# Kernel tuning notes

Measured on AMD Instinct MI355X. Metric: run time of the kernel, lower is better.

Reference implementation:

```python
import jax, jax.numpy as jnp
import numpy as np

FISTA_ITER = 50
LAMBDA = 0.1
POWER_ITER = 100


def power_method(W):
    # Estimates c = largest eigenvalue of W^T W (squared spectral norm).
    # Torch code uses a random init vector; we use a fixed key for determinism.
    X0 = jax.random.normal(jax.random.key(1), (1, W.shape[1]), dtype=W.dtype)

    def body(i, carry):
        X, _ = carry
        X = (X @ W.T) @ W            # [1, m]
        nm = jnp.linalg.norm(X)
        return (X / nm, nm)

    _, nm = jax.lax.fori_loop(0, POWER_ITER, body, (X0, jnp.asarray(1.0, W.dtype)))
    return nm


def soft_threshold(X, lam):
    return jnp.sign(X) * jax.nn.relu(jnp.abs(X) - lam)


def fista(Y, W, lam, iters):
    c = power_method(W)
    eta = 1.0 / c
    Gamma0 = soft_threshold(Y @ (eta * W), lam)   # [B, m]
    Y_norm = jnp.linalg.norm(Y)
    t0 = jnp.asarray(1.0, Y.dtype)

    def step(carry, _):
        Gamma, Z, t = carry
        residual = Z @ W.T - Y                                   # [B, n]
        Gamma_new = soft_threshold(Z - eta * (residual @ W), lam / c)
        t_new = (1.0 + jnp.sqrt(1.0 + 4.0 * t ** 2)) / 2.0
        Z_new = Gamma_new + (t - 1.0) / t_new * (Gamma_new - Gamma)
        nrm = jnp.linalg.norm(residual) / Y_norm
        return (Gamma_new, Z_new, t_new), nrm

    (Gamma, _, _), norms = jax.lax.scan(step, (Gamma0, Gamma0, t0), None, length=iters)
    return Gamma, norms


def setup_inputs() -> dict:
    key = jax.random.key(0)
    k1, k2 = jax.random.split(key)
    Y = jax.random.normal(k1, (8192, 784), dtype=jnp.float32)
    W = jax.random.normal(k2, (784, 2048), dtype=jnp.float32)
    W = W / jnp.linalg.norm(W, axis=0, keepdims=True)  # NormDict
    return {"Y": Y, "W": W}


def reference(Y, W):
    Gamma, norms = fista(Y, W, LAMBDA, FISTA_ITER)
    X = Gamma @ W.T                  # reconstruction [B, 784]
    return (X, Gamma, norms)
```

## Files before the change

### kernel.cpp

```cpp
#include <hip/hip_runtime.h>
#include <math.h>

#define B_DIM   8192
#define N_DIM   784
#define NPAD    800
#define NROWS_W 1024
#define M_DIM   2048
#define XSZ     (B_DIM*N_DIM)
#define GSZ     (B_DIM*M_DIM)
#define NITER   50
#define PITER   100

typedef __attribute__((ext_vector_type(8))) short short8;
typedef __attribute__((ext_vector_type(4))) float floatx4;

__device__ __forceinline__ void async_ld16(const unsigned short* g, unsigned short* l){
  __builtin_amdgcn_global_load_lds(
      (const __attribute__((address_space(1))) unsigned int*)g,
      (__attribute__((address_space(3))) unsigned int*)l,
      16, 0, 0);
}

__device__ __forceinline__ unsigned rotl32(unsigned x, int d){ return (x<<d)|(x>>(32-d)); }

__device__ void threefry2x32(unsigned& v0, unsigned& v1){
  const unsigned ks0=0u, ks1=1u, ks2=0x1BD11BDBu;
  unsigned x0=v0+ks0, x1=v1+ks1;
#define RND(R) { x0+=x1; x1=rotl32(x1,R); x1^=x0; }
  RND(13) RND(15) RND(26) RND(6)
  x0+=ks1; x1+=ks2+1u;
  RND(17) RND(29) RND(16) RND(24)
  x0+=ks2; x1+=ks0+2u;
  RND(13) RND(15) RND(26) RND(6)
  x0+=ks0; x1+=ks1+3u;
  RND(17) RND(29) RND(16) RND(24)
  x0+=ks1; x1+=ks2+4u;
  RND(13) RND(15) RND(26) RND(6)
  x0+=ks2; x1+=ks0+5u;
#undef RND
  v0=x0; v1=x1;
}

__device__ float erfinv_f(float x){
  float w = -logf((1.0f-x)*(1.0f+x));
  float p;
  if (w < 5.0f){
    w -= 2.5f;
    p = 2.81022636e-08f;
    p = fmaf(p,w, 3.43273939e-07f);
    p = fmaf(p,w,-3.5233877e-06f);
    p = fmaf(p,w,-4.39150654e-06f);
    p = fmaf(p,w, 0.00021858087f);
    p = fmaf(p,w,-0.00125372503f);
    p = fmaf(p,w,-0.00417768164f);
    p = fmaf(p,w, 0.246640727f);
    p = fmaf(p,w, 1.50140941f);
  } else {
    w = sqrtf(w) - 3.0f;
    p = -0.000200214257f;
    p = fmaf(p,w, 0.000100950558f);
    p = fmaf(p,w, 0.00134934322f);
    p = fmaf(p,w,-0.00367342844f);
    p = fmaf(p,w, 0.00573950773f);
    p = fmaf(p,w,-0.0076224613f);
    p = fmaf(p,w, 0.00943887047f);
    p = fmaf(p,w, 1.00167406f);
    p = fmaf(p,w, 2.83297682f);
  }
  return p*x;
}

__device__ float bits_to_normal(unsigned b){
  unsigned fb = (b>>9) | 0x3f800000u;
  float u01 = __uint_as_float(fb) - 1.0f;
  const float lo = -0.99999994f;
  float u = u01*(1.0f - lo) + lo;
  u = fmaxf(lo, u);
  return 1.41421356237f * erfinv_f(u);
}

__global__ void setup_kernel(float* __restrict__ xbuf0, float* __restrict__ accs,
                             float* __restrict__ dbuf){
  int i = threadIdx.x;
  if (i < 64) accs[i] = 0.0f;
  if (i < 128) dbuf[i] = (i==0) ? 1.0f : 0.0f;
  unsigned v0 = (unsigned)i, v1 = (unsigned)(1024+i);
  threefry2x32(v0, v1);
  xbuf0[i]        = bits_to_normal(v0);
  xbuf0[1024 + i] = bits_to_normal(v1);
}

__device__ __forceinline__ unsigned short f2bf(float f){
  unsigned u = __float_as_uint(f);
  unsigned r = (u + 0x7fffu + ((u>>16)&1u)) >> 16;
  return (unsigned short)r;
}
__device__ __forceinline__ unsigned pack2(float a, float b){
  return (unsigned)f2bf(a) | ((unsigned)f2bf(b) << 16);
}
__device__ __forceinline__ float bf2f(unsigned short s){
  return __uint_as_float(((unsigned)s) << 16);
}

__global__ void conv_w(const float* __restrict__ W, unsigned short* __restrict__ Wbf){
  int i4 = (blockIdx.x*256 + threadIdx.x)*4;
  int row = i4 >> 11;
  uint2 p = make_uint2(0,0);
  if (row < N_DIM){
    float4 v = *(const float4*)(W + (size_t)row*M_DIM + (i4 & 2047));
    p.x = pack2(v.x, v.y); p.y = pack2(v.z, v.w);
  }
  *(uint2*)(Wbf + i4) = p;
}

__global__ void conv_y(const float* __restrict__ Y, unsigned short* __restrict__ Ybf){
  int row = blockIdx.x;
  int c4 = threadIdx.x*4;
  if (c4 >= NPAD) return;
  uint2 p = make_uint2(0,0);
  if (c4 < N_DIM){
    float4 v = *(const float4*)(Y + (size_t)row*N_DIM + c4);
    p.x = pack2(v.x, v.y); p.y = pack2(v.z, v.w);
  }
  *(uint2*)(Ybf + (size_t)row*NPAD + c4) = p;
}

__global__ void transpose_w(const float* __restrict__ W, unsigned short* __restrict__ WTbf){
  __shared__ float tile[32][33];
  int k0 = blockIdx.x*32;
  int j0 = blockIdx.y*32;
  int tx = threadIdx.x & 31, ty = threadIdx.x >> 5;
#pragma unroll
  for (int i=0;i<4;i++){
    int j = j0 + ty + 8*i;
    float v = (j < N_DIM) ? W[(size_t)j*M_DIM + k0 + tx] : 0.0f;
    tile[tx][ty+8*i] = v;
  }
  __syncthreads();
#pragma unroll
  for (int i=0;i<4;i++){
    int k = k0 + ty + 8*i;
    WTbf[(size_t)k*NPAD + j0 + tx] = f2bf(tile[ty+8*i][tx]);
  }
}

__global__ __launch_bounds__(256)
void compute_qp(const float* __restrict__ W, float* __restrict__ Qp){
  __shared__ float As2[64][33];
  __shared__ float Bs2[64][33];
  const int t = threadIdx.x;
  const int a0 = blockIdx.x*64, b0 = blockIdx.y*64;
  const int ty = t>>4, tx = t&15;
  float acc[4][4];
#pragma unroll
  for (int i=0;i<4;i++)
#pragma unroll
    for (int j=0;j<4;j++) acc[i][j]=0.0f;

  for (int k0=0; k0<M_DIM; k0+=32){
#pragma unroll
    for (int h=0; h<2; ++h){
      int row = h*32 + (t>>3);
      int kq  = (t&7)*4;
      float4 av = make_float4(0,0,0,0), bv = make_float4(0,0,0,0);
      if (a0+row < N_DIM) av = *(const float4*)(W + (size_t)(a0+row)*M_DIM + k0 + kq);
      if (b0+row < N_DIM) bv = *(const float4*)(W + (size_t)(b0+row)*M_DIM + k0 + kq);
      As2[row][kq]=av.x; As2[row][kq+1]=av.y; As2[row][kq+2]=av.z; As2[row][kq+3]=av.w;
      Bs2[row][kq]=bv.x; Bs2[row][kq+1]=bv.y; Bs2[row][kq+2]=bv.z; Bs2[row][kq+3]=bv.w;
    }
    __syncthreads();
#pragma unroll
    for (int kk=0; kk<32; ++kk){
      float a[4], b[4];
#pragma unroll
      for (int i=0;i<4;i++) a[i] = As2[ty*4+i][kk];
#pragma unroll
      for (int j=0;j<4;j++) b[j] = Bs2[tx*4+j][kk];
#pragma unroll
      for (int i=0;i<4;i++)
#pragma unroll
        for (int j=0;j<4;j++) acc[i][j] = fmaf(a[i], b[j], acc[i][j]);
    }
    __syncthreads();
  }
#pragma unroll
  for (int i=0;i<4;i++){
    int a = a0 + ty*4 + i;
    if (a >= N_DIM) continue;
#pragma unroll
    for (int j=0;j<4;j++){
      int b = b0 + tx*4 + j;
      if (b < N_DIM) Qp[(size_t)a*N_DIM + b] = acc[i][j];
    }
  }
}

__global__ void u0_kernel(const float* __restrict__ x0, const float* __restrict__ W,
                          float* __restrict__ u0){
  int wave = threadIdx.x>>6, lane = threadIdx.x&63;
  int j = blockIdx.x*4 + wave;
  const float* Wr = W + (size_t)j*M_DIM;
  float s = 0.0f;
  for (int k=lane; k<M_DIM; k+=64) s = fmaf(x0[k], Wr[k], s);
  for (int off=32; off>0; off>>=1) s += __shfl_down(s, off);
  if (lane==0) u0[j] = s;
}

__global__ void pm_qp(const float* __restrict__ vin, const float* __restrict__ din,
                      const float* __restrict__ Qp,
                      float* __restrict__ vout, float* __restrict__ dout){
  int wave = threadIdx.x>>6, lane = threadIdx.x&63;
  int j = blockIdx.x*4 + wave;
  float inv = 1.0f/sqrtf(*din);
  const float* Qr = Qp + (size_t)j*N_DIM;
  float s = 0.0f;
  for (int k=lane; k<N_DIM; k+=64) s = fmaf(vin[k], Qr[k], s);
  for (int off=32; off>0; off>>=1) s += __shfl_down(s, off);
  if (lane==0){
    float w = s * inv;
    vout[j] = w;
    atomicAdd(dout, w * vin[j] * inv);
  }
}

__global__ void finish_power2(const float* __restrict__ d100, const float* __restrict__ accs,
                              float* __restrict__ params){
  float c = sqrtf(*d100);
  params[0] = c;
  params[1] = 1.0f/c;
  params[2] = 0.1f/c;
  params[3] = sqrtf(accs[0]);
}

__global__ void sumsq_kernel(const float* __restrict__ v, int n, float* __restrict__ acc){
  __shared__ float red[256];
  int t = threadIdx.x;
  float s = 0.0f;
  for (int i = blockIdx.x*256 + t; i < n; i += gridDim.x*256){ float x = v[i]; s = fmaf(x,x,s); }
  red[t] = s; __syncthreads();
  for (int off=128; off>0; off>>=1){ if (t<off) red[t]+=red[t+off]; __syncthreads(); }
  if (t==0) atomicAdd(acc, red[0]);
}

__device__ __forceinline__ float softthr(float v, float th){
  float a = fmaxf(fabsf(v) - th, 0.0f);
  return copysignf(a, v);
}

template<int MODE>
__global__ __launch_bounds__(256)
void mfma_nt(const unsigned short* __restrict__ Abf,
             const unsigned short* __restrict__ Bbf,
             const float* __restrict__ Y,
             unsigned short* __restrict__ Rbf,
             float* __restrict__ X,
             float* __restrict__ nacc){
  __shared__ float4 smem4[2560];
  unsigned short* As0 = (unsigned short*)smem4;
  unsigned short* Bs0 = As0 + 64*32;
  unsigned short* As1 = Bs0 + 256*32;
  unsigned short* Bs1 = As1 + 64*32;
  float* fbuf = (float*)smem4;

  const int bid = blockIdx.x;
  const int g8  = bid & 7, w = bid >> 3;
  const int m0  = (g8*16 + (w>>2))*64;
  const int n0  = (w & 3)*256;

  const int t    = threadIdx.x;
  const int wave = t>>6, lane = t&63;
  const int wm2  = wave>>1, wn2 = wave&1;
  const int quad = lane>>4, l15 = lane&15;
  const int lrow = lane>>2;
  const int lks  = ((lane&3) ^ ((lrow>>1)&3))*8;
  const int ksw  = (quad ^ ((l15>>1)&3))*8;

  floatx4 acc[2][8];
#pragma unroll
  for (int i=0;i<2;i++)
#pragma unroll
    for (int j=0;j<8;j++) acc[i][j] = (floatx4)(0.0f);

  auto stage = [&](unsigned short* As, unsigned short* Bs, int k0){
    async_ld16(Abf + (size_t)(m0 + wave*16 + lrow)*M_DIM + k0 + lks, &As[wave*512]);
#pragma unroll
    for (int c=0; c<4; ++c){
      int chunk = wave*4 + c;
      async_ld16(Bbf + (size_t)(n0 + chunk*16 + lrow)*M_DIM + k0 + lks, &Bs[chunk*512]);
    }
  };

  stage(As0, Bs0, 0);
  __syncthreads();
  int cur = 0;
  for (int k0=0; k0<M_DIM; k0+=32, cur^=1){
    unsigned short* As = cur ? As1 : As0;
    unsigned short* Bs = cur ? Bs1 : Bs0;
    if (k0+32 < M_DIM) stage(cur ? As0 : As1, cur ? Bs0 : Bs1, k0+32);
    short8 af[2], bfr[8];
#pragma unroll
    for (int ti=0; ti<2; ++ti)
      af[ti] = *(const short8*)&As[(wm2*32 + ti*16 + l15)*32 + ksw];
#pragma unroll
    for (int tj=0; tj<8; ++tj)
      bfr[tj] = *(const short8*)&Bs[(wn2*128 + tj*16 + l15)*32 + ksw];
#pragma unroll
    for (int ti=0; ti<2; ++ti)
#pragma unroll
      for (int tj=0; tj<8; ++tj)
        acc[ti][tj] = __builtin_amdgcn_mfma_f32_16x16x32_bf16(af[ti], bfr[tj], acc[ti][tj], 0, 0, 0);
    __syncthreads();
  }

  float ss = 0.0f;
#pragma unroll
  for (int c=0; c<4; ++c){
    if (wn2 == (c>>1)){
      int tb = (c&1)*4;
#pragma unroll
      for (int ti=0; ti<2; ++ti)
#pragma unroll
        for (int u=0; u<4; ++u)
#pragma unroll
          for (int r=0; r<4; ++r)
            fbuf[(wm2*32 + ti*16 + quad*4 + r)*68 + u*16 + l15] = acc[ti][tb+u][r];
    }
    __syncthreads();
#pragma unroll
    for (int k=0; k<4; ++k){
      int row = k*16 + (t>>4);
      int col = (t&15)*4;
      int m = m0 + row;
      int n = n0 + c*64 + col;
      float4 v = *(const float4*)&fbuf[row*68 + col];
      if (MODE==0){
        if (n < N_DIM){
          float4 yv = *(const float4*)(Y + (size_t)m*N_DIM + n);
          float r0 = v.x - yv.x, r1 = v.y - yv.y, r2 = v.z - yv.z, r3 = v.w - yv.w;
          uint2 p; p.x = pack2(r0, r1); p.y = pack2(r2, r3);
          *(uint2*)(Rbf + (size_t)m*NPAD + n) = p;
          ss = fmaf(r0,r0, fmaf(r1,r1, fmaf(r2,r2, fmaf(r3,r3, ss))));
        } else if (n < NPAD){
          *(uint2*)(Rbf + (size_t)m*NPAD + n) = make_uint2(0,0);
        }
      } else {
        if (n < N_DIM) *(float4*)(X + (size_t)m*N_DIM + n) = v;
      }
    }
    __syncthreads();
  }

  if (MODE==0){
    for (int off=32; off>0; off>>=1) ss += __shfl_down(ss, off);
    if (lane==0) atomicAdd(nacc, ss);
  }
}

template<int MODE>
__global__ __launch_bounds__(256,3)
void mfma_nn(const unsigned short* __restrict__ Abf,
             const unsigned short* __restrict__ WTbf,
             float* __restrict__ Gamma,
             unsigned short* __restrict__ Zhi,
             float* __restrict__ Zf,
             float* __restrict__ Gf,
             const float* __restrict__ params,
             float mu){
  __shared__ float4 smem4[2048];
  unsigned short* As0 = (unsigned short*)smem4;
  unsigned short* Bs0 = As0 + 128*32;
  unsigned short* As1 = Bs0 + 128*32;
  unsigned short* Bs1 = As1 + 128*32;
  float* fbuf = (float*)smem4;

  const int bid = blockIdx.x;
  const int g8  = bid & 7, w = bid >> 3;
  const int m0  = (g8*8 + (w>>4))*128;
  const int n0  = (w & 15)*128;

  const int t    = threadIdx.x;
  const int wave = t>>6, lane = t&63;
  const int wm   = wave>>1, wn = wave&1;
  const int quad = lane>>4, l15 = lane&15;
  const int lrow = lane>>2;
  const int lks  = ((lane&3) ^ ((lrow>>1)&3))*8;
  const int ksw  = (quad ^ ((l15>>1)&3))*8;

  floatx4 acc[4][4];
#pragma unroll
  for (int i=0;i<4;i++)
#pragma unroll
    for (int j=0;j<4;j++) acc[i][j] = (floatx4)(0.0f);

  auto stage = [&](unsigned short* As, unsigned short* Bs, int k0){
#pragma unroll
    for (int c=0; c<2; ++c){
      int chunk = wave*2 + c;
      async_ld16(Abf  + (size_t)(m0 + chunk*16 + lrow)*NPAD + k0 + lks, &As[chunk*512]);
      async_ld16(WTbf + (size_t)(n0 + chunk*16 + lrow)*NPAD + k0 + lks, &Bs[chunk*512]);
    }
  };

  stage(As0, Bs0, 0);
  __syncthreads();
  int cur = 0;
  for (int k0=0; k0<NPAD; k0+=32, cur^=1){
    unsigned short* As = cur ? As1 : As0;
    unsigned short* Bs = cur ? Bs1 : Bs0;
    if (k0+32 < NPAD) stage(cur ? As0 : As1, cur ? Bs0 : Bs1, k0+32);
    short8 af[4], bfr[4];
#pragma unroll
    for (int ti=0; ti<4; ++ti)
      af[ti] = *(const short8*)&As[(wm*64 + ti*16 + l15)*32 + ksw];
#pragma unroll
    for (int tj=0; tj<4; ++tj)
      bfr[tj] = *(const short8*)&Bs[(wn*64 + tj*16 + l15)*32 + ksw];
#pragma unroll
    for (int ti=0; ti<4; ++ti)
#pragma unroll
      for (int tj=0; tj<4; ++tj)
        acc[ti][tj] = __builtin_amdgcn_mfma_f32_16x16x32_bf16(af[ti], bfr[tj], acc[ti][tj], 0, 0, 0);
    __syncthreads();
  }

  const float eta  = params[1];
  const float lamc = params[2];
  const size_t blockL = (size_t)((m0>>7)*16 + (n0>>7));
  float* GfB = Gf + blockL*16384 + (size_t)t*4;
  float* ZfB = Zf + blockL*16384 + (size_t)t*4;
  const int mrow0 = m0 + wm*64 + quad*4;
  const int ncol  = n0 + wn*64 + l15;

  if (MODE==2){
#pragma unroll
    for (int ti=0; ti<4; ++ti)
#pragma unroll
      for (int tj=0; tj<4; ++tj){
        float4 zf4 = *(const float4*)(ZfB + (ti*4+tj)*1024);
        acc[ti][tj][0] = softthr(zf4.x - eta*acc[ti][tj][0], lamc);
        acc[ti][tj][1] = softthr(zf4.y - eta*acc[ti][tj][1], lamc);
        acc[ti][tj][2] = softthr(zf4.z - eta*acc[ti][tj][2], lamc);
        acc[ti][tj][3] = softthr(zf4.w - eta*acc[ti][tj][3], lamc);
      }
    __syncthreads();
#pragma unroll
    for (int c=0; c<4; ++c){
      if (wn == (c>>1)){
        int tb = (c&1)*2;
#pragma unroll
        for (int ti=0; ti<4; ++ti)
#pragma unroll
          for (int u=0; u<2; ++u)
#pragma unroll
            for (int r=0; r<4; ++r)
              fbuf[(wm*64 + ti*16 + quad*4 + r)*36 + u*16 + l15] = acc[ti][tb+u][r];
      }
      __syncthreads();
#pragma unroll
      for (int k=0; k<4; ++k){
        int row = k*32 + (t>>3);
        int col = (t&7)*4;
        int m = m0 + row;
        int n = n0 + c*32 + col;
        size_t idx = (size_t)m*M_DIM + n;
        float4 g4 = *(const float4*)&fbuf[row*36 + col];
        *(float4*)(Gamma + idx) = g4;
        uint2 phx; phx.x = pack2(g4.x, g4.y); phx.y = pack2(g4.z, g4.w);
        *(uint2*)(Zhi + idx) = phx;
      }
      __syncthreads();
    }
  } else {
#pragma unroll
    for (int ti=0; ti<4; ++ti){
      float4 go4[4], zf4[4];
      if (MODE==1){
#pragma unroll
        for (int tj=0; tj<4; ++tj) go4[tj] = *(const float4*)(GfB + (ti*4+tj)*1024);
#pragma unroll
        for (int tj=0; tj<4; ++tj) zf4[tj] = *(const float4*)(ZfB + (ti*4+tj)*1024);
      }
#pragma unroll
      for (int tj=0; tj<4; ++tj){
        float gr[4], zn[4];
        if (MODE==1){
          float z[4]  = {zf4[tj].x, zf4[tj].y, zf4[tj].z, zf4[tj].w};
          float go[4] = {go4[tj].x, go4[tj].y, go4[tj].z, go4[tj].w};
#pragma unroll
          for (int r=0;r<4;r++){
            gr[r] = softthr(z[r] - eta*acc[ti][tj][r], lamc);
            zn[r] = gr[r] + mu*(gr[r] - go[r]);
          }
        } else {
#pragma unroll
          for (int r=0;r<4;r++){ gr[r] = softthr(eta*acc[ti][tj][r], 0.1f); zn[r] = gr[r]; }
        }
        *(float4*)(GfB + (ti*4+tj)*1024) = make_float4(gr[0],gr[1],gr[2],gr[3]);
        *(float4*)(ZfB + (ti*4+tj)*1024) = make_float4(zn[0],zn[1],zn[2],zn[3]);
        size_t zb = (size_t)(mrow0 + ti*16)*M_DIM + ncol + tj*16;
        Zhi[zb]            = f2bf(zn[0]);
        Zhi[zb + M_DIM]    = f2bf(zn[1]);
        Zhi[zb + 2*M_DIM]  = f2bf(zn[2]);
        Zhi[zb + 3*M_DIM]  = f2bf(zn[3]);
      }
    }
  }
}

__global__ void norms_finalize(const float* __restrict__ nacc, const float* __restrict__ params,
                               float* __restrict__ out){
  int i = threadIdx.x;
  if (i < NITER) out[i] = sqrtf(nacc[i]) / params[3];
}

extern "C" void kernel_launch(void* const* d_in, const int* in_sizes, int n_in,
                              void* d_out, int out_size, void* d_ws, size_t ws_size,
                              hipStream_t stream){
  const float* Y  = (const float*)d_in[0];
  const float* W  = (const float*)d_in[1];
  float* out      = (float*)d_out;
  float* X        = out;
  float* Gamma    = out + XSZ;
  float* norms    = out + XSZ + GSZ;

  unsigned short* Zhi  = (unsigned short*)d_ws;
  float* Zf            = (float*)(Zhi + (size_t)GSZ);
  unsigned short* Rbf  = (unsigned short*)(Zf + (size_t)GSZ);
  unsigned short* Wbf  = Rbf  + (size_t)B_DIM*NPAD;
  unsigned short* WTbf = Wbf  + (size_t)NROWS_W*M_DIM;
  float* Qp     = (float*)(WTbf + (size_t)M_DIM*NPAD);
  float* w0     = Qp + (size_t)N_DIM*N_DIM;
  float* w1     = w0 + 1024;
  float* dbuf   = w1 + 1024;
  float* params = dbuf + 128;
  float* accs   = params + 8;
  float* xb0    = accs + 64;

  float* Gf = Gamma;

  setup_kernel<<<dim3(1), dim3(1024), 0, stream>>>(xb0, accs, dbuf);
  sumsq_kernel<<<dim3(512), dim3(256), 0, stream>>>(Y, XSZ, accs);
  conv_w      <<<dim3(2048), dim3(256), 0, stream>>>(W, Wbf);
  transpose_w <<<dim3(64,25), dim3(256), 0, stream>>>(W, WTbf);
  conv_y      <<<dim3(B_DIM), dim3(256), 0, stream>>>(Y, Rbf);

  compute_qp<<<dim3(13,13), dim3(256), 0, stream>>>(W, Qp);
  u0_kernel <<<dim3(196), dim3(256), 0, stream>>>(xb0, W, w0);
  float* va = w0; float* vb = w1;
  for (int it=1; it<=PITER; ++it){
    pm_qp<<<dim3(196), dim3(256), 0, stream>>>(va, dbuf + it - 1, Qp, vb, dbuf + it);
    float* tmp = va; va = vb; vb = tmp;
  }
  finish_power2<<<dim3(1), dim3(1), 0, stream>>>(dbuf + PITER, accs, params);

  mfma_nn<0><<<dim3(1024), dim3(256), 0, stream>>>(Rbf, WTbf, Gamma, Zhi, Zf, Gf, params, 0.0f);

  float tcur = 1.0f;
  for (int it=0; it<NITER; ++it){
    mfma_nt<0><<<dim3(512), dim3(256), 0, stream>>>(Zhi, Wbf, Y, Rbf, nullptr, accs + 1 + it);
    float tsq = tcur*tcur;
    float tn  = (1.0f + sqrtf(1.0f + 4.0f*tsq)) / 2.0f;
    float mu  = (tcur - 1.0f) / tn;
    tcur = tn;
    if (it < NITER-1)
      mfma_nn<1><<<dim3(1024), dim3(256), 0, stream>>>(Rbf, WTbf, Gamma, Zhi, Zf, Gf, params, mu);
    else
      mfma_nn<2><<<dim3(1024), dim3(256), 0, stream>>>(Rbf, WTbf, Gamma, Zhi, Zf, Gf, params, mu);
  }

  norms_finalize<<<dim3(1), dim3(64), 0, stream>>>(accs + 1, params, norms);

  mfma_nt<1><<<dim3(512), dim3(256), 0, stream>>>(Zhi, Wbf, nullptr, nullptr, X, nullptr);
}
```

Measured before the change: 8.931 ms.

## Store Z as bf16 hi/lo pair and split-K the W·Wᵀ Gram kernel

The FISTA update kernel stops keeping a full fp32 copy of Z in a blocked workspace. It stores Z as two bf16 arrays (a high part and a residual low part) and reconstructs fp32 values by adding them. The epilogue now goes through LDS in every mode, giving coalesced row-major reads of Gamma and Z, and it drops the strided scalar bf16 stores. This reduces per-iteration HBM traffic for Z, at the cost of slightly lower precision for Z (roughly 16 mantissa bits). Separately, the Gram-matrix kernel is split 8-way along K and accumulates with atomics after a new zeroing kernel, which raises parallelism in a small setup step.

```diff
diff --git a/kernel.cpp b/kernel.cpp
--- a/kernel.cpp
+++ b/kernel.cpp
@@ -144,12 +144,23 @@
   }
 }
 
+__global__ void zero_qp(float* __restrict__ Qp){
+  int i = (blockIdx.x*256 + threadIdx.x)*4;
+  if (i < N_DIM*N_DIM){
+    Qp[i] = 0.0f;
+    if (i+1 < N_DIM*N_DIM) Qp[i+1] = 0.0f;
+    if (i+2 < N_DIM*N_DIM) Qp[i+2] = 0.0f;
+    if (i+3 < N_DIM*N_DIM) Qp[i+3] = 0.0f;
+  }
+}
+
 __global__ __launch_bounds__(256)
 void compute_qp(const float* __restrict__ W, float* __restrict__ Qp){
   __shared__ float As2[64][33];
   __shared__ float Bs2[64][33];
   const int t = threadIdx.x;
   const int a0 = blockIdx.x*64, b0 = blockIdx.y*64;
+  const int kbase = blockIdx.z*256;
   const int ty = t>>4, tx = t&15;
   float acc[4][4];
 #pragma unroll
@@ -157,7 +168,7 @@
 #pragma unroll
     for (int j=0;j<4;j++) acc[i][j]=0.0f;
 
-  for (int k0=0; k0<M_DIM; k0+=32){
+  for (int k0=kbase; k0<kbase+256; k0+=32){
 #pragma unroll
     for (int h=0; h<2; ++h){
       int row = h*32 + (t>>3);
@@ -190,7 +201,7 @@
 #pragma unroll
     for (int j=0;j<4;j++){
       int b = b0 + tx*4 + j;
-      if (b < N_DIM) Qp[(size_t)a*N_DIM + b] = acc[i][j];
+      if (b < N_DIM) atomicAdd(&Qp[(size_t)a*N_DIM + b], acc[i][j]);
     }
   }
 }
@@ -362,8 +373,7 @@
              const unsigned short* __restrict__ WTbf,
              float* __restrict__ Gamma,
              unsigned short* __restrict__ Zhi,
-             float* __restrict__ Zf,
-             float* __restrict__ Gf,
+             unsigned short* __restrict__ Zlo,
              const float* __restrict__ params,
              float mu){
   __shared__ float4 smem4[2048];
@@ -425,85 +435,82 @@
 
   const float eta  = params[1];
   const float lamc = params[2];
-  const size_t blockL = (size_t)((m0>>7)*16 + (n0>>7));
-  float* GfB = Gf + blockL*16384 + (size_t)t*4;
-  float* ZfB = Zf + blockL*16384 + (size_t)t*4;
-  const int mrow0 = m0 + wm*64 + quad*4;
-  const int ncol  = n0 + wn*64 + l15;
-
-  if (MODE==2){
-#pragma unroll
-    for (int ti=0; ti<4; ++ti)
-#pragma unroll
-      for (int tj=0; tj<4; ++tj){
-        float4 zf4 = *(const float4*)(ZfB + (ti*4+tj)*1024);
-        acc[ti][tj][0] = softthr(zf4.x - eta*acc[ti][tj][0], lamc);
-        acc[ti][tj][1] = softthr(zf4.y - eta*acc[ti][tj][1], lamc);
-        acc[ti][tj][2] = softthr(zf4.z - eta*acc[ti][tj][2], lamc);
-        acc[ti][tj][3] = softthr(zf4.w - eta*acc[ti][tj][3], lamc);
+
+#pragma unroll
+  for (int c=0; c<4; ++c){
+    if (wn == (c>>1)){
+      int tb = (c&1)*2;
+#pragma unroll
+      for (int ti=0; ti<4; ++ti)
+#pragma unroll
+        for (int u=0; u<2; ++u)
+#pragma unroll
+          for (int r=0; r<4; ++r)
+            fbuf[(wm*64 + ti*16 + quad*4 + r)*36 + u*16 + l15] = acc[ti][tb+u][r];
+    }
+    __syncthreads();
+    const int rbase = t>>3;
+    const int col   = (t&7)*4;
+    const int n     = n0 + c*32 + col;
+    size_t idx[4];
+    uint2 ph[4], pl[4];
+    float4 gov[4];
+#pragma unroll
+    for (int k=0; k<4; ++k){
+      int m = m0 + k*32 + rbase;
+      idx[k] = (size_t)m*M_DIM + n;
+      if (MODE!=0){
+        ph[k] = *(const uint2*)(Zhi + idx[k]);
+        pl[k] = *(const uint2*)(Zlo + idx[k]);
       }
-    __syncthreads();
-#pragma unroll
-    for (int c=0; c<4; ++c){
-      if (wn == (c>>1)){
-        int tb = (c&1)*2;
-#pragma unroll
-        for (int ti=0; ti<4; ++ti)
-#pragma unroll
-          for (int u=0; u<2; ++u)
-#pragma unroll
-            for (int r=0; r<4; ++r)
-              fbuf[(wm*64 + ti*16 + quad*4 + r)*36 + u*16 + l15] = acc[ti][tb+u][r];
+      if (MODE==1) gov[k] = *(const float4*)(Gamma + idx[k]);
+    }
+#pragma unroll
+    for (int k=0; k<4; ++k){
+      int row = k*32 + rbase;
+      float4 g4 = *(const float4*)&fbuf[row*36 + col];
+      float gr[4] = {g4.x, g4.y, g4.z, g4.w};
+      if (MODE!=0){
+        unsigned short h[4] = {(unsigned short)(ph[k].x&0xffff),(unsigned short)(ph[k].x>>16),
+                               (unsigned short)(ph[k].y&0xffff),(unsigned short)(ph[k].y>>16)};
+        unsigned short l[4] = {(unsigned short)(pl[k].x&0xffff),(unsigned short)(pl[k].x>>16),
+                               (unsigned short)(pl[k].y&0xffff),(unsigned short)(pl[k].y>>16)};
+#pragma unroll
+        for (int e=0;e<4;e++){
+          float zv = bf2f(h[e]) + bf2f(l[e]);
+          gr[e] = softthr(zv - eta*gr[e], lamc);
+        }
+      } else {
+#pragma unroll
+        for (int e=0;e<4;e++) gr[e] = softthr(eta*gr[e], 0.1f);
       }
-      __syncthreads();
-#pragma unroll
-      for (int k=0; k<4; ++k){
-        int row = k*32 + (t>>3);
-        int col = (t&7)*4;
-        int m = m0 + row;
-        int n = n0 + c*32 + col;
-        size_t idx = (size_t)m*M_DIM + n;
-        float4 g4 = *(const float4*)&fbuf[row*36 + col];
-        *(float4*)(Gamma + idx) = g4;
-        uint2 phx; phx.x = pack2(g4.x, g4.y); phx.y = pack2(g4.z, g4.w);
-        *(uint2*)(Zhi + idx) = phx;
+      *(float4*)(Gamma + idx[k]) = make_float4(gr[0],gr[1],gr[2],gr[3]);
+      if (MODE==1){
+        float go0 = gov[k].x, go1 = gov[k].y, go2 = gov[k].z, go3 = gov[k].w;
+        float zn[4];
+        zn[0] = gr[0] + mu*(gr[0] - go0);
+        zn[1] = gr[1] + mu*(gr[1] - go1);
+        zn[2] = gr[2] + mu*(gr[2] - go2);
+        zn[3] = gr[3] + mu*(gr[3] - go3);
+        unsigned short h0=f2bf(zn[0]), h1=f2bf(zn[1]), h2=f2bf(zn[2]), h3=f2bf(zn[3]);
+        uint2 phx; phx.x = (unsigned)h0 | ((unsigned)h1<<16); phx.y = (unsigned)h2 | ((unsigned)h3<<16);
+        uint2 plx; plx.x = pack2(zn[0]-bf2f(h0), zn[1]-bf2f(h1));
+                   plx.y = pack2(zn[2]-bf2f(h2), zn[3]-bf2f(h3));
+        *(uint2*)(Zhi + idx[k]) = phx;
+        *(uint2*)(Zlo + idx[k]) = plx;
+      } else if (MODE==0){
+        unsigned short h0=f2bf(gr[0]), h1=f2bf(gr[1]), h2=f2bf(gr[2]), h3=f2bf(gr[3]);
+        uint2 phx; phx.x = (unsigned)h0 | ((unsigned)h1<<16); phx.y = (unsigned)h2 | ((unsigned)h3<<16);
+        uint2 plx; plx.x = pack2(gr[0]-bf2f(h0), gr[1]-bf2f(h1));
+                   plx.y = pack2(gr[2]-bf2f(h2), gr[3]-bf2f(h3));
+        *(uint2*)(Zhi + idx[k]) = phx;
+        *(uint2*)(Zlo + idx[k]) = plx;
+      } else {
+        uint2 phx; phx.x = pack2(gr[0], gr[1]); phx.y = pack2(gr[2], gr[3]);
+        *(uint2*)(Zhi + idx[k]) = phx;
       }
-      __syncthreads();
-    }
-  } else {
-#pragma unroll
-    for (int ti=0; ti<4; ++ti){
-      float4 go4[4], zf4[4];
-      if (MODE==1){
-#pragma unroll
-        for (int tj=0; tj<4; ++tj) go4[tj] = *(const float4*)(GfB + (ti*4+tj)*1024);
-#pragma unroll
-        for (int tj=0; tj<4; ++tj) zf4[tj] = *(const float4*)(ZfB + (ti*4+tj)*1024);
-      }
-#pragma unroll
-      for (int tj=0; tj<4; ++tj){
-        float gr[4], zn[4];
-        if (MODE==1){
-          float z[4]  = {zf4[tj].x, zf4[tj].y, zf4[tj].z, zf4[tj].w};
-          float go[4] = {go4[tj].x, go4[tj].y, go4[tj].z, go4[tj].w};
-#pragma unroll
-          for (int r=0;r<4;r++){
-            gr[r] = softthr(z[r] - eta*acc[ti][tj][r], lamc);
-            zn[r] = gr[r] + mu*(gr[r] - go[r]);
-          }
-        } else {
-#pragma unroll
-          for (int r=0;r<4;r++){ gr[r] = softthr(eta*acc[ti][tj][r], 0.1f); zn[r] = gr[r]; }
-        }
-        *(float4*)(GfB + (ti*4+tj)*1024) = make_float4(gr[0],gr[1],gr[2],gr[3]);
-        *(float4*)(ZfB + (ti*4+tj)*1024) = make_float4(zn[0],zn[1],zn[2],zn[3]);
-        size_t zb = (size_t)(mrow0 + ti*16)*M_DIM + ncol + tj*16;
-        Zhi[zb]            = f2bf(zn[0]);
-        Zhi[zb + M_DIM]    = f2bf(zn[1]);
-        Zhi[zb + 2*M_DIM]  = f2bf(zn[2]);
-        Zhi[zb + 3*M_DIM]  = f2bf(zn[3]);
-      }
-    }
+    }
+    __syncthreads();
   }
 }
 
@@ -524,8 +531,8 @@
   float* norms    = out + XSZ + GSZ;
 
   unsigned short* Zhi  = (unsigned short*)d_ws;
-  float* Zf            = (float*)(Zhi + (size_t)GSZ);
-  unsigned short* Rbf  = (unsigned short*)(Zf + (size_t)GSZ);
+  unsigned short* Zlo  = Zhi  + (size_t)GSZ;
+  unsigned short* Rbf  = Zlo  + (size_t)GSZ;
   unsigned short* Wbf  = Rbf  + (size_t)B_DIM*NPAD;
   unsigned short* WTbf = Wbf  + (size_t)NROWS_W*M_DIM;
   float* Qp     = (float*)(WTbf + (size_t)M_DIM*NPAD);
@@ -536,15 +543,14 @@
   float* accs   = params + 8;
   float* xb0    = accs + 64;
 
-  float* Gf = Gamma;
-
   setup_kernel<<<dim3(1), dim3(1024), 0, stream>>>(xb0, accs, dbuf);
   sumsq_kernel<<<dim3(512), dim3(256), 0, stream>>>(Y, XSZ, accs);
   conv_w      <<<dim3(2048), dim3(256), 0, stream>>>(W, Wbf);
   transpose_w <<<dim3(64,25), dim3(256), 0, stream>>>(W, WTbf);
   conv_y      <<<dim3(B_DIM), dim3(256), 0, stream>>>(Y, Rbf);
 
-  compute_qp<<<dim3(13,13), dim3(256), 0, stream>>>(W, Qp);
+  zero_qp   <<<dim3(601), dim3(256), 0, stream>>>(Qp);
+  compute_qp<<<dim3(13,13,8), dim3(256), 0, stream>>>(W, Qp);
   u0_kernel <<<dim3(196), dim3(256), 0, stream>>>(xb0, W, w0);
   float* va = w0; float* vb = w1;
   for (int it=1; it<=PITER; ++it){
@@ -553,7 +559,7 @@
   }
   finish_power2<<<dim3(1), dim3(1), 0, stream>>>(dbuf + PITER, accs, params);
 
-  mfma_nn<0><<<dim3(1024), dim3(256), 0, stream>>>(Rbf, WTbf, Gamma, Zhi, Zf, Gf, params, 0.0f);
+  mfma_nn<0><<<dim3(1024), dim3(256), 0, stream>>>(Rbf, WTbf, Gamma, Zhi, Zlo, params, 0.0f);
 
   float tcur = 1.0f;
   for (int it=0; it<NITER; ++it){
@@ -563,9 +569,9 @@
     float mu  = (tcur - 1.0f) / tn;
     tcur = tn;
     if (it < NITER-1)
-      mfma_nn<1><<<dim3(1024), dim3(256), 0, stream>>>(Rbf, WTbf, Gamma, Zhi, Zf, Gf, params, mu);
+      mfma_nn<1><<<dim3(1024), dim3(256), 0, stream>>>(Rbf, WTbf, Gamma, Zhi, Zlo, params, mu);
     else
-      mfma_nn<2><<<dim3(1024), dim3(256), 0, stream>>>(Rbf, WTbf, Gamma, Zhi, Zf, Gf, params, mu);
+      mfma_nn<2><<<dim3(1024), dim3(256), 0, stream>>>(Rbf, WTbf, Gamma, Zhi, Zlo, params, mu);
   }
 
   norms_finalize<<<dim3(1), dim3(64), 0, stream>>>(accs + 1, params, norms);
```

After: 9.207 ms. +3.1%, slower.
